# Optimization experiments

Hardware: AMD Instinct MI355X
Metric: run time of the kernel (lower is better)

Reference implementation:

```python
import jax, jax.numpy as jnp
import numpy as np

B, NK, NQ = 16, 1024, 1024
D_IN, D_V, D_H = 3, 8, 128
NUGGET = 1e-3   # diagonal regularizer for the kriging covariance solve
EPS = 1e-12     # keeps sqrt differentiable at zero distance


def _mlp(x, w1, b1, w2, b2, w3, b3):
    # Linear -> ReLU -> Linear -> ReLU -> Linear (torch Linear: y = x @ W.T + b)
    h = jax.nn.relu(x @ w1.T + b1)
    h = jax.nn.relu(h @ w2.T + b2)
    return h @ w3.T + b3


def _cdist(a, b):
    # a: [B,N,D], b: [B,M,D] -> [B,N,M] Euclidean distances
    d2 = (jnp.sum(a * a, -1)[:, :, None]
          + jnp.sum(b * b, -1)[:, None, :]
          - 2.0 * jnp.einsum('bnd,bmd->bnm', a, b))
    return jnp.sqrt(jnp.maximum(d2, 0.0) + EPS)


def _linear_init(key, out_f, in_f):
    k1, k2 = jax.random.split(key)
    lim = 1.0 / np.sqrt(in_f)
    w = jax.random.uniform(k1, (out_f, in_f), jnp.float32, -lim, lim)
    b = jax.random.uniform(k2, (out_f,), jnp.float32, -lim, lim)
    return w, b


def setup_inputs() -> dict:
    key = jax.random.key(0)
    ks = jax.random.split(key, 10)
    KEY = jax.random.normal(ks[0], (B, NK, D_IN), jnp.float32)
    VALUE = jax.random.normal(ks[1], (B, NK, D_V), jnp.float32)
    QUERY = jax.random.normal(ks[2], (B, NQ, D_IN), jnp.float32)
    W1_w, W1_b = _linear_init(ks[3], D_H, D_IN)
    W2_w, W2_b = _linear_init(ks[4], D_H, D_H)
    W3_w, W3_b = _linear_init(ks[5], D_IN, D_H)
    Wv1_w, Wv1_b = _linear_init(ks[6], D_H, D_V)
    Wv2_w, Wv2_b = _linear_init(ks[7], D_H, D_H)
    Wv3_w, Wv3_b = _linear_init(ks[8], D_V, D_H)
    return dict(KEY=KEY, VALUE=VALUE, QUERY=QUERY,
                W1_w=W1_w, W1_b=W1_b, W2_w=W2_w, W2_b=W2_b, W3_w=W3_w, W3_b=W3_b,
                Wv1_w=Wv1_w, Wv1_b=Wv1_b, Wv2_w=Wv2_w, Wv2_b=Wv2_b, Wv3_w=Wv3_w, Wv3_b=Wv3_b)


def reference(KEY, VALUE, QUERY,
              W1_w, W1_b, W2_w, W2_b, W3_w, W3_b,
              Wv1_w, Wv1_b, Wv2_w, Wv2_b, Wv3_w, Wv3_b):
    # shared MLP on KEY and QUERY, separate MLP on VALUE
    Wk = _mlp(KEY, W1_w, W1_b, W2_w, W2_b, W3_w, W3_b)
    Wq = _mlp(QUERY, W1_w, W1_b, W2_w, W2_b, W3_w, W3_b)
    Wv = _mlp(VALUE, Wv1_w, Wv1_b, Wv2_w, Wv2_b, Wv3_w, Wv3_b)
    VALUE_scale = VALUE * Wv                  # einsum('bij,bij->bij')
    # kriging prediction with learned elementwise coordinate scalings
    Ks = KEY * Wk                             # [B,NK,D_IN]
    Qs = QUERY * Wq                           # [B,NQ,D_IN]
    C_kk = jnp.exp(-_cdist(Ks, Ks)) + NUGGET * jnp.eye(NK, dtype=KEY.dtype)  # [B,NK,NK]
    C_qk = jnp.exp(-_cdist(Qs, Ks))                                          # [B,NQ,NK]
    # kriging weights: solve C_kk @ lam = C_qk^T  -> lam [B,NK,NQ]
    lam = jnp.linalg.solve(C_kk, jnp.swapaxes(C_qk, 1, 2))
    # prediction: weighted sum of scaled values -> [B,NQ,D_V]
    return jnp.einsum('bkq,bkv->bqv', lam, VALUE_scale)
```

## Files before the change

kernel.cpp:

```cpp
#include <hip/hip_runtime.h>
#include <hip/hip_bf16.h>


__device__ __forceinline__ int row_of(int e) {
    int i = (int)((sqrtf(8.0f * (float)e + 1.0f) - 1.0f) * 0.5f);
    while ((i + 1) * (i + 2) / 2 <= e) i++;
    while (i * (i + 1) / 2 > e) i--;
    return i;
}

__global__ void k_transpose(const float* __restrict__ W2, const float* __restrict__ Wv2,
                            float* __restrict__ W2T, float* __restrict__ Wv2T) {
    int tid = blockIdx.x * 256 + threadIdx.x;
    int e = tid & 16383;
    int r = e >> 7, c = e & 127;
    if (tid < 16384) W2T[c * 128 + r] = W2[e];
    else             Wv2T[c * 128 + r] = Wv2[e];
}

template<int DI, int P>
__device__ __forceinline__ void mlp_body(const float* __restrict__ in,
                                         float* __restrict__ out, int base,
                                         const float* __restrict__ W1,
                                         const float* __restrict__ b1,
                                         const float* __restrict__ W2T,
                                         const float* __restrict__ b2,
                                         const float* __restrict__ W3,
                                         const float* __restrict__ b3) {
    __shared__ float xs[P][DI];
    __shared__ float h1[P][128];
    __shared__ float h2[P][129];
    int t = threadIdx.x;
    for (int i = t; i < P * DI; i += 128) xs[i / DI][i % DI] = in[base * DI + i];
    __syncthreads();
    float w1r[DI];
#pragma unroll
    for (int d = 0; d < DI; d++) w1r[d] = W1[t * DI + d];
    float b1t = b1[t], b2t = b2[t];
#pragma unroll
    for (int p = 0; p < P; p++) {
        float s = b1t;
#pragma unroll
        for (int d = 0; d < DI; d++) s += w1r[d] * xs[p][d];
        h1[p][t] = fmaxf(s, 0.0f);
    }
    __syncthreads();
    float acc[P];
#pragma unroll
    for (int p = 0; p < P; p++) acc[p] = b2t;
    for (int k = 0; k < 128; k++) {
        float w = W2T[k * 128 + t];
#pragma unroll
        for (int p = 0; p < P; p++) acc[p] += w * h1[p][k];
    }
#pragma unroll
    for (int p = 0; p < P; p++) h2[p][t] = fmaxf(acc[p], 0.0f);
    __syncthreads();
    if (t < P * DI) {
        int p = t / DI, d = t % DI;
        float s = b3[d];
        for (int k = 0; k < 128; k++) s += W3[d * 128 + k] * h2[p][k];
        int gi = base * DI + t;
        out[gi] = in[gi] * s;
    }
}

__global__ void k_mlp_kq(const float* __restrict__ KEY, float* __restrict__ Ks,
                         const float* __restrict__ QUERY, float* __restrict__ Qs,
                         const float* __restrict__ W1, const float* __restrict__ b1,
                         const float* __restrict__ W2T, const float* __restrict__ b2,
                         const float* __restrict__ W3, const float* __restrict__ b3) {
    if (blockIdx.x < 512)
        mlp_body<3, 32>(KEY, Ks, blockIdx.x * 32, W1, b1, W2T, b2, W3, b3);
    else
        mlp_body<3, 32>(QUERY, Qs, (blockIdx.x - 512) * 32, W1, b1, W2T, b2, W3, b3);
}

__global__ void k_mlp_v(const float* __restrict__ VALUE, float* __restrict__ Vs,
                        const float* __restrict__ W1, const float* __restrict__ b1,
                        const float* __restrict__ W2T, const float* __restrict__ b2,
                        const float* __restrict__ W3, const float* __restrict__ b3) {
    mlp_body<8, 16>(VALUE, Vs, blockIdx.x * 16, W1, b1, W2T, b2, W3, b3);
}

__global__ void k_buildC(const float* __restrict__ Ks, float* __restrict__ C) {
    long idx = (long)blockIdx.x * 256 + threadIdx.x;
    int b = (int)(idx >> 20);
    int rem = (int)(idx & 1048575);
    int i = rem >> 10, j = rem & 1023;
    const float* a = Ks + ((long)b * 1024 + i) * 3;
    const float* bb = Ks + ((long)b * 1024 + j) * 3;
    float d0 = a[0] - bb[0], d1 = a[1] - bb[1], d2 = a[2] - bb[2];
    float dist = sqrtf(d0 * d0 + d1 * d1 + d2 * d2 + 1e-12f);
    float v = __expf(-dist);
    if (i == j) v += 1e-3f;
    C[idx] = v;
}

__device__ void potf_body(float* __restrict__ C, float* __restrict__ V,
                          int o, int last, int b) {
    int tid = threadIdx.x;
    float* A = C + (long)b * 1048576;
    float* Vp = V + (long)b * 8192;
    __shared__ float T[128][132];
    __shared__ __align__(16) float cv[128][8];
    __shared__ __align__(16) float cw[128][8];
    __shared__ __align__(16) float Pn[128][8];
    __shared__ __align__(16) float St[32][132];
    __shared__ float rsd[128];
    __shared__ float W[32][33];
    __shared__ float zs[128][9];
    bool active = (tid < 136);
    int ti = 0, tj = 0;
    if (active) { ti = row_of(tid); tj = tid - ti * (ti + 1) / 2; }
    int r0 = ti * 8, c0t = tj * 8;
    float Treg[8][8];
    if (active) {
        const float* src = A + (long)(o + r0) * 1024 + o + c0t;
#pragma unroll
        for (int i = 0; i < 8; i++) {
            float4 va = *(const float4*)(src + (long)i * 1024);
            float4 vb = *(const float4*)(src + (long)i * 1024 + 4);
            Treg[i][0] = va.x; Treg[i][1] = va.y; Treg[i][2] = va.z; Treg[i][3] = va.w;
            Treg[i][4] = vb.x; Treg[i][5] = vb.y; Treg[i][6] = vb.z; Treg[i][7] = vb.w;
        }
    }
    int lane = tid & 63;
    __syncthreads();
    if (o > 0) {
        for (int kc = 0; kc < 4; kc++) {
            {
                int r = tid >> 1, lk = (tid & 1) * 16;
                const float* sp = A + (long)(o + r) * 1024 + (o - 128) + kc * 32 + lk;
#pragma unroll
                for (int k4 = 0; k4 < 4; k4++) {
                    float4 v = *(const float4*)(sp + 4 * k4);
                    St[lk + 4*k4    ][r] = v.x;
                    St[lk + 4*k4 + 1][r] = v.y;
                    St[lk + 4*k4 + 2][r] = v.z;
                    St[lk + 4*k4 + 3][r] = v.w;
                }
            }
            __syncthreads();
            if (active) {
#pragma unroll 4
                for (int k = 0; k < 32; k++) {
                    float4 a0 = *(const float4*)&St[k][r0];
                    float4 a1 = *(const float4*)&St[k][r0 + 4];
                    float4 b0 = *(const float4*)&St[k][c0t];
                    float4 b1 = *(const float4*)&St[k][c0t + 4];
                    float aa[8] = {a0.x,a0.y,a0.z,a0.w,a1.x,a1.y,a1.z,a1.w};
                    float bb[8] = {b0.x,b0.y,b0.z,b0.w,b1.x,b1.y,b1.z,b1.w};
#pragma unroll
                    for (int i = 0; i < 8; i++)
#pragma unroll
                        for (int j = 0; j < 8; j++) Treg[i][j] -= aa[i] * bb[j];
                }
            }
            __syncthreads();
        }
    }
    for (int jbt = 0; jbt < 16; jbt++) {
        int jb = jbt * 8;
        if (active && tj == jbt) {
#pragma unroll
            for (int i = 0; i < 8; i++) {
                *(float4*)&Pn[r0 + i][0] = make_float4(Treg[i][0], Treg[i][1], Treg[i][2], Treg[i][3]);
                *(float4*)&Pn[r0 + i][4] = make_float4(Treg[i][4], Treg[i][5], Treg[i][6], Treg[i][7]);
            }
        }
        __syncthreads();
        if (tid < 64) {
            int r1 = lane, r2 = 64 + lane;
            float v1[8], v2[8], w1[8], w2[8];
#pragma unroll
            for (int q = 0; q < 8; q++) {
                int j = jb + q;
                int jl = j & 63;
                bool hi = (j >= 64);
                float a1 = Pn[r1][q], a2 = Pn[r2][q];
#pragma unroll
                for (int p = 0; p < 8; p++) {
                    if (p < q) {
                        float wj = __shfl(hi ? w2[p] : w1[p], jl);
                        a1 -= v1[p] * wj;
                        a2 -= v2[p] * wj;
                    }
                }
                v1[q] = a1; v2[q] = a2;
                float dj = __shfl(hi ? a2 : a1, jl);
                float dinv = 1.0f / dj;
                w1[q] = a1 * dinv; w2[q] = a2 * dinv;
            }
            *(float4*)&cv[r1][0] = make_float4(v1[0], v1[1], v1[2], v1[3]);
            *(float4*)&cv[r1][4] = make_float4(v1[4], v1[5], v1[6], v1[7]);
            *(float4*)&cv[r2][0] = make_float4(v2[0], v2[1], v2[2], v2[3]);
            *(float4*)&cv[r2][4] = make_float4(v2[4], v2[5], v2[6], v2[7]);
            *(float4*)&cw[r1][0] = make_float4(w1[0], w1[1], w1[2], w1[3]);
            *(float4*)&cw[r1][4] = make_float4(w1[4], w1[5], w1[6], w1[7]);
            *(float4*)&cw[r2][0] = make_float4(w2[0], w2[1], w2[2], w2[3]);
            *(float4*)&cw[r2][4] = make_float4(w2[4], w2[5], w2[6], w2[7]);
        }
        __syncthreads();
        if (active && tj == jbt) {
#pragma unroll
            for (int i = 0; i < 8; i++) {
                float4 va = *(const float4*)&cv[r0 + i][0];
                float4 vb = *(const float4*)&cv[r0 + i][4];
                Treg[i][0] = va.x; Treg[i][1] = va.y; Treg[i][2] = va.z; Treg[i][3] = va.w;
                Treg[i][4] = vb.x; Treg[i][5] = vb.y; Treg[i][6] = vb.z; Treg[i][7] = vb.w;
            }
        } else if (active && tj > jbt) {
#pragma unroll
            for (int h = 0; h < 2; h++) {
                float va4[8][4], wb4[8][4];
#pragma unroll
                for (int i = 0; i < 8; i++) {
                    float4 v = *(const float4*)&cv[r0 + i][h * 4];
                    va4[i][0] = v.x; va4[i][1] = v.y; va4[i][2] = v.z; va4[i][3] = v.w;
                }
#pragma unroll
                for (int j = 0; j < 8; j++) {
                    float4 v = *(const float4*)&cw[c0t + j][h * 4];
                    wb4[j][0] = v.x; wb4[j][1] = v.y; wb4[j][2] = v.z; wb4[j][3] = v.w;
                }
#pragma unroll
                for (int i = 0; i < 8; i++)
#pragma unroll
                    for (int j = 0; j < 8; j++)
                        Treg[i][j] -= va4[i][0] * wb4[j][0] + va4[i][1] * wb4[j][1]
                                    + va4[i][2] * wb4[j][2] + va4[i][3] * wb4[j][3];
            }
        }
        __syncthreads();
    }
    if (active) {
#pragma unroll
        for (int i = 0; i < 8; i++) {
            *(float4*)&T[r0 + i][c0t]     = make_float4(Treg[i][0], Treg[i][1], Treg[i][2], Treg[i][3]);
            *(float4*)&T[r0 + i][c0t + 4] = make_float4(Treg[i][4], Treg[i][5], Treg[i][6], Treg[i][7]);
        }
    }
    __syncthreads();
    int rg = tid >> 4;
    int cg = tid & 15;
    int wv = tid >> 6;
    if (tid < 128) rsd[tid] = rsqrtf(T[tid][tid]);
    __syncthreads();
#pragma unroll
    for (int j = 0; j < 8; j++) {
        int c = cg + 16 * j;
#pragma unroll
        for (int i = 0; i < 8; i++) {
            int r = rg * 8 + i;
            if (c <= r) T[r][c] *= rsd[c];
            else        T[r][c] = 0.0f;
        }
    }
    __syncthreads();
    if (lane < 32) {
        int d0 = wv * 32;
        int j = lane;
        float x[32];
#pragma unroll
        for (int i = 0; i < 32; i++) {
            float dinv = 1.0f / T[d0 + i][d0 + i];
            float s = 0.0f;
#pragma unroll
            for (int k = 0; k < i; k++) s += T[d0 + i][d0 + k] * x[k];
            x[i] = (i == j) ? dinv : -s * dinv;
        }
#pragma unroll
        for (int i = 0; i < 32; i++) T[d0 + i][d0 + j] = x[i];
    }
    __syncthreads();
    int orr = tid >> 3;
    int oc = (tid & 7) * 4;
    for (int j = 0; j < 3; j++) {
        for (int i = j + 1; i < 4; i++) {
            float w0 = 0, w1 = 0, w2 = 0, w3 = 0;
            for (int kb = j; kb < i; kb++) {
#pragma unroll 8
                for (int kk = 0; kk < 32; kk++) {
                    float l = T[i * 32 + orr][kb * 32 + kk];
                    w0 += l * T[kb * 32 + kk][j * 32 + oc    ];
                    w1 += l * T[kb * 32 + kk][j * 32 + oc + 1];
                    w2 += l * T[kb * 32 + kk][j * 32 + oc + 2];
                    w3 += l * T[kb * 32 + kk][j * 32 + oc + 3];
                }
            }
            W[orr][oc] = w0; W[orr][oc+1] = w1; W[orr][oc+2] = w2; W[orr][oc+3] = w3;
            __syncthreads();
            float v0 = 0, v1 = 0, v2 = 0, v3 = 0;
#pragma unroll 8
            for (int kk = 0; kk < 32; kk++) {
                float l = T[i * 32 + orr][i * 32 + kk];
                v0 += l * W[kk][oc    ];
                v1 += l * W[kk][oc + 1];
                v2 += l * W[kk][oc + 2];
                v3 += l * W[kk][oc + 3];
            }
            __syncthreads();
            T[i * 32 + orr][j * 32 + oc    ] = -v0;
            T[i * 32 + orr][j * 32 + oc + 1] = -v1;
            T[i * 32 + orr][j * 32 + oc + 2] = -v2;
            T[i * 32 + orr][j * 32 + oc + 3] = -v3;
            __syncthreads();
        }
    }
    {
        int r = tid >> 1, c0 = (tid & 1) * 64;
        float* dst = A + (long)(o + r) * 1024 + o + c0;
#pragma unroll
        for (int k = 0; k < 16; k++) {
            int c = c0 + 4 * k;
            float4 v = make_float4(T[r][c], T[r][c + 1], T[r][c + 2], T[r][c + 3]);
            *(float4*)(dst + 4 * k) = v;
        }
    }
    {
        int k = tid >> 1, c0 = (tid & 1) * 4;
        float4 v = *(const float4*)&Vp[(o + k) * 8 + c0];
        zs[k][c0] = v.x; zs[k][c0 + 1] = v.y; zs[k][c0 + 2] = v.z; zs[k][c0 + 3] = v.w;
    }
    __syncthreads();
    {
        int r = tid & 127, c0 = (tid >> 7) * 4;
        float y0 = 0, y1 = 0, y2 = 0, y3 = 0;
#pragma unroll 8
        for (int k = 0; k < 128; k++) {
            float l = T[r][k];
            y0 += l * zs[k][c0    ];
            y1 += l * zs[k][c0 + 1];
            y2 += l * zs[k][c0 + 2];
            y3 += l * zs[k][c0 + 3];
        }
        if (!last) {
            *(float4*)&Vp[(o + r) * 8 + c0] = make_float4(y0, y1, y2, y3);
        } else {
            __syncthreads();
            zs[r][c0] = y0; zs[r][c0+1] = y1; zs[r][c0+2] = y2; zs[r][c0+3] = y3;
            __syncthreads();
            float x0 = 0, x1 = 0, x2 = 0, x3 = 0;
#pragma unroll 8
            for (int k = 0; k < 128; k++) {
                float l = T[k][r];
                x0 += l * zs[k][c0    ];
                x1 += l * zs[k][c0 + 1];
                x2 += l * zs[k][c0 + 2];
                x3 += l * zs[k][c0 + 3];
            }
            *(float4*)&Vp[(o + r) * 8 + c0] = make_float4(x0, x1, x2, x3);
        }
    }
}

__device__ void syrk_body(float* __restrict__ C, int o, int pti, int ptj, int b) {
    float* A = C + (long)b * 1048576;
    int bi = o + 128 + pti * 128, bj = o + 128 + ptj * 128;
    __shared__ float As[32][132];
    __shared__ float Bs[32][132];
    int tid = threadIdx.x;
    int tx = tid & 15, ty = tid >> 4;
    float acc[8][8] = {};
    int lr = tid >> 1;
    int lk = (tid & 1) * 16;
    bool diag = (bi == bj);
    for (int kc = 0; kc < 128; kc += 32) {
        {
            const float* src = A + (long)(bi + lr) * 1024 + o + kc + lk;
#pragma unroll
            for (int k4 = 0; k4 < 4; k4++) {
                float4 v = *(const float4*)(src + 4 * k4);
                As[lk + 4*k4    ][lr] = v.x;
                As[lk + 4*k4 + 1][lr] = v.y;
                As[lk + 4*k4 + 2][lr] = v.z;
                As[lk + 4*k4 + 3][lr] = v.w;
            }
            if (!diag) {
                const float* sb = A + (long)(bj + lr) * 1024 + o + kc + lk;
#pragma unroll
                for (int k4 = 0; k4 < 4; k4++) {
                    float4 v = *(const float4*)(sb + 4 * k4);
                    Bs[lk + 4*k4    ][lr] = v.x;
                    Bs[lk + 4*k4 + 1][lr] = v.y;
                    Bs[lk + 4*k4 + 2][lr] = v.z;
                    Bs[lk + 4*k4 + 3][lr] = v.w;
                }
            }
        }
        __syncthreads();
        {
            const float (*Bp)[132] = diag ? As : Bs;
#pragma unroll
            for (int k = 0; k < 32; k++) {
                float4 a0 = *(const float4*)&As[k][ty * 8];
                float4 a1 = *(const float4*)&As[k][ty * 8 + 4];
                float4 b0 = *(const float4*)&Bp[k][tx * 8];
                float4 b1 = *(const float4*)&Bp[k][tx * 8 + 4];
                float aa[8] = {a0.x,a0.y,a0.z,a0.w,a1.x,a1.y,a1.z,a1.w};
                float bb[8] = {b0.x,b0.y,b0.z,b0.w,b1.x,b1.y,b1.z,b1.w};
#pragma unroll
                for (int i = 0; i < 8; i++)
#pragma unroll
                    for (int j = 0; j < 8; j++) acc[i][j] += aa[i] * bb[j];
            }
        }
        __syncthreads();
    }
#pragma unroll
    for (int i = 0; i < 8; i++) {
        int r = bi + ty * 8 + i;
        float* dst = A + (long)r * 1024 + bj + tx * 8;
        if (!diag) {
            float4 p0 = *(const float4*)dst;
            float4 p1 = *(const float4*)(dst + 4);
            p0.x -= acc[i][0]; p0.y -= acc[i][1]; p0.z -= acc[i][2]; p0.w -= acc[i][3];
            p1.x -= acc[i][4]; p1.y -= acc[i][5]; p1.z -= acc[i][6]; p1.w -= acc[i][7];
            *(float4*)dst = p0;
            *(float4*)(dst + 4) = p1;
        } else {
#pragma unroll
            for (int j = 0; j < 8; j++) {
                int c = bj + tx * 8 + j;
                if (c <= r) dst[j] -= acc[i][j];
            }
        }
    }
}

__global__ __launch_bounds__(256) void k_potf_syrk(float* __restrict__ C,
                                                   float* __restrict__ V,
                                                   int o, int last) {
    int bx = blockIdx.x;
    if (bx < 16) {
        potf_body(C, V, o, last, bx);
    } else {
        int v = bx - 16;
        int bb = v & 15;
        int p = (v >> 4) + 1;
        int tii = row_of(p);
        int tjj = p - tii * (tii + 1) / 2;
        syrk_body(C, o - 128, tii, tjj, bb);
    }
}

__global__ __launch_bounds__(256) void k_trsmg(float* __restrict__ C,
                                               float* __restrict__ V, int o) {
    int b = blockIdx.y;
    float* A = C + (long)b * 1048576;
    float* Vp = V + (long)b * 8192;
    int bi = o + 128 + blockIdx.x * 128;
    const float* Linv = A + (long)o * 1024 + o;
    __shared__ float As[32][132];
    __shared__ float Ls[32][132];
    int tid = threadIdx.x;
    int tx = tid & 15, ty = tid >> 4;
    float acc[8][8] = {};
    int lr = tid >> 1;
    int lk = (tid & 1) * 16;
    for (int kc = 0; kc < 128; kc += 32) {
        const float* src = A + (long)(bi + lr) * 1024 + o + kc + lk;
        const float* sl  = Linv + (long)lr * 1024 + kc + lk;
#pragma unroll
        for (int k4 = 0; k4 < 4; k4++) {
            float4 v = *(const float4*)(src + 4 * k4);
            As[lk + 4*k4    ][lr] = v.x;
            As[lk + 4*k4 + 1][lr] = v.y;
            As[lk + 4*k4 + 2][lr] = v.z;
            As[lk + 4*k4 + 3][lr] = v.w;
            float4 w = *(const float4*)(sl + 4 * k4);
            Ls[lk + 4*k4    ][lr] = w.x;
            Ls[lk + 4*k4 + 1][lr] = w.y;
            Ls[lk + 4*k4 + 2][lr] = w.z;
            Ls[lk + 4*k4 + 3][lr] = w.w;
        }
        __syncthreads();
#pragma unroll
        for (int k = 0; k < 32; k++) {
            float4 a0 = *(const float4*)&As[k][ty * 8];
            float4 a1 = *(const float4*)&As[k][ty * 8 + 4];
            float4 b0 = *(const float4*)&Ls[k][tx * 8];
            float4 b1 = *(const float4*)&Ls[k][tx * 8 + 4];
            float aa[8] = {a0.x,a0.y,a0.z,a0.w,a1.x,a1.y,a1.z,a1.w};
            float bb[8] = {b0.x,b0.y,b0.z,b0.w,b1.x,b1.y,b1.z,b1.w};
#pragma unroll
            for (int i = 0; i < 8; i++)
#pragma unroll
                for (int j = 0; j < 8; j++) acc[i][j] += aa[i] * bb[j];
        }
        __syncthreads();
    }
#pragma unroll
    for (int i = 0; i < 8; i++) {
        float* dst = A + (long)(bi + ty * 8 + i) * 1024 + o + tx * 8;
        *(float4*)dst       = make_float4(acc[i][0], acc[i][1], acc[i][2], acc[i][3]);
        *(float4*)(dst + 4) = make_float4(acc[i][4], acc[i][5], acc[i][6], acc[i][7]);
    }
    float* ysf = &Ls[0][0];
    {
        int k = tid >> 1, c0 = (tid & 1) * 4;
        float4 v = *(const float4*)&Vp[(o + k) * 8 + c0];
        ysf[k * 9 + c0] = v.x; ysf[k * 9 + c0 + 1] = v.y;
        ysf[k * 9 + c0 + 2] = v.z; ysf[k * 9 + c0 + 3] = v.w;
    }
    __syncthreads();
    float zacc0 = 0, zacc1 = 0, zacc2 = 0, zacc3 = 0;
    int zr = tid & 127, zc0 = (tid >> 7) * 4;
#pragma unroll
    for (int ch = 0; ch < 4; ch++) {
        if ((tx >> 2) == ch) {
            int cb = (tx & 3) * 8;
#pragma unroll
            for (int j = 0; j < 8; j++)
#pragma unroll
                for (int i = 0; i < 8; i++)
                    As[cb + j][ty * 8 + i] = acc[i][j];
        }
        __syncthreads();
#pragma unroll 8
        for (int k = 0; k < 32; k++) {
            float l = As[k][zr];
            const float* yp = &ysf[(ch * 32 + k) * 9 + zc0];
            zacc0 += l * yp[0]; zacc1 += l * yp[1];
            zacc2 += l * yp[2]; zacc3 += l * yp[3];
        }
        __syncthreads();
    }
    float* vp = &Vp[(bi + zr) * 8 + zc0];
    float4 old = *(const float4*)vp;
    old.x -= zacc0; old.y -= zacc1; old.z -= zacc2; old.w -= zacc3;
    *(float4*)vp = old;
}

__global__ __launch_bounds__(256) void k_bstep(const float* __restrict__ C,
                                               float* __restrict__ V, int k) {
    int b = blockIdx.y, j = blockIdx.x, tid = threadIdx.x;
    const float* A = C + (long)b * 1048576;
    float* Vp = V + (long)b * 8192;
    __shared__ float Lb[128][129];
    __shared__ float xs[128][9];
    __shared__ float ys[128][9];
    {
        int kk = tid >> 1, c0 = (tid & 1) * 4;
        float4 v = *(const float4*)&Vp[(k * 128 + kk) * 8 + c0];
        xs[kk][c0] = v.x; xs[kk][c0+1] = v.y; xs[kk][c0+2] = v.z; xs[kk][c0+3] = v.w;
    }
#pragma unroll
    for (int m = 0; m < 16; m++) {
        int e = tid + m * 256;
        int i = e >> 5, j4 = (e & 31) * 4;
        float4 v = *(const float4*)&A[(long)(k * 128 + i) * 1024 + j * 128 + j4];
        Lb[i][j4] = v.x; Lb[i][j4+1] = v.y; Lb[i][j4+2] = v.z; Lb[i][j4+3] = v.w;
    }
    __syncthreads();
    int r = tid & 127, c0 = (tid >> 7) * 4;
    float u0 = 0, u1 = 0, u2 = 0, u3 = 0;
#pragma unroll 8
    for (int kk = 0; kk < 128; kk++) {
        float l = Lb[kk][r];
        u0 += l * xs[kk][c0    ];
        u1 += l * xs[kk][c0 + 1];
        u2 += l * xs[kk][c0 + 2];
        u3 += l * xs[kk][c0 + 3];
    }
    float* vp = &Vp[(j * 128 + r) * 8 + c0];
    float4 old = *(const float4*)vp;
    old.x -= u0; old.y -= u1; old.z -= u2; old.w -= u3;
    if (j < k - 1) {
        *(float4*)vp = old;
    } else {
        ys[r][c0] = old.x; ys[r][c0+1] = old.y; ys[r][c0+2] = old.z; ys[r][c0+3] = old.w;
        __syncthreads();
        int o = j * 128;
#pragma unroll
        for (int m = 0; m < 16; m++) {
            int e = tid + m * 256;
            int i = e >> 5, j4 = (e & 31) * 4;
            float4 v = *(const float4*)&A[(long)(o + i) * 1024 + o + j4];
            Lb[i][j4] = v.x; Lb[i][j4+1] = v.y; Lb[i][j4+2] = v.z; Lb[i][j4+3] = v.w;
        }
        __syncthreads();
        float x0 = 0, x1 = 0, x2 = 0, x3 = 0;
#pragma unroll 8
        for (int kk = 0; kk < 128; kk++) {
            float l = Lb[kk][r];
            x0 += l * ys[kk][c0    ];
            x1 += l * ys[kk][c0 + 1];
            x2 += l * ys[kk][c0 + 2];
            x3 += l * ys[kk][c0 + 3];
        }
        *(float4*)vp = make_float4(x0, x1, x2, x3);
    }
}

__global__ void k_out(const float* __restrict__ Qs, const float* __restrict__ Ks,
                      const float* __restrict__ X, float* __restrict__ out) {
    int b = blockIdx.x >> 4;
    int qc = blockIdx.x & 15;
    int t = threadIdx.x;
    int q = t & 63, ks = t >> 6;
    __shared__ float kx[1024][3];
    __shared__ __align__(16) float xv[1024][8];
    __shared__ float red[4][64][8];
    for (int i = t; i < 3072; i += 256) kx[i / 3][i % 3] = Ks[b * 3072 + i];
    for (int i = t; i < 8192; i += 256) xv[i >> 3][i & 7] = X[b * 8192 + i];
    __syncthreads();
    int gq = b * 1024 + qc * 64 + q;
    const float* qp = Qs + (long)gq * 3;
    float qx = qp[0], qy = qp[1], qz = qp[2];
    float acc[8] = {};
    int k0 = ks * 256;
#pragma unroll 2
    for (int k = k0; k < k0 + 256; k++) {
        float dx = qx - kx[k][0], dy = qy - kx[k][1], dz = qz - kx[k][2];
        float w = __expf(-sqrtf(dx * dx + dy * dy + dz * dz + 1e-12f));
        float4 xa = *(const float4*)&xv[k][0];
        float4 xb = *(const float4*)&xv[k][4];
        acc[0] += w * xa.x; acc[1] += w * xa.y; acc[2] += w * xa.z; acc[3] += w * xa.w;
        acc[4] += w * xb.x; acc[5] += w * xb.y; acc[6] += w * xb.z; acc[7] += w * xb.w;
    }
#pragma unroll
    for (int c = 0; c < 8; c++) red[ks][q][c] = acc[c];
    __syncthreads();
    if (ks == 0) {
        float* op = out + (long)gq * 8;
#pragma unroll
        for (int c = 0; c < 8; c++)
            op[c] = red[0][q][c] + red[1][q][c] + red[2][q][c] + red[3][q][c];
    }
}

extern "C" void kernel_launch(void* const* d_in, const int* in_sizes, int n_in,
                              void* d_out, int out_size, void* d_ws, size_t ws_size,
                              hipStream_t stream) {
    const float* KEY   = (const float*)d_in[0];
    const float* VALUE = (const float*)d_in[1];
    const float* QUERY = (const float*)d_in[2];
    const float* W1w = (const float*)d_in[3];  const float* W1b = (const float*)d_in[4];
    const float* W2w = (const float*)d_in[5];  const float* W2b = (const float*)d_in[6];
    const float* W3w = (const float*)d_in[7];  const float* W3b = (const float*)d_in[8];
    const float* Wv1w = (const float*)d_in[9]; const float* Wv1b = (const float*)d_in[10];
    const float* Wv2w = (const float*)d_in[11];const float* Wv2b = (const float*)d_in[12];
    const float* Wv3w = (const float*)d_in[13];const float* Wv3b = (const float*)d_in[14];

    float* ws  = (float*)d_ws;
    float* C    = ws;
    float* Ks   = C + 16777216;
    float* Qs   = Ks + 49152;
    float* Vs   = Qs + 49152;
    float* W2T  = Vs + 131072;
    float* Wv2T = W2T + 16384;

    float* out = (float*)d_out;

    hipLaunchKernelGGL(k_transpose, dim3(128), dim3(256), 0, stream, W2w, Wv2w, W2T, Wv2T);
    hipLaunchKernelGGL(k_mlp_kq, dim3(1024), dim3(128), 0, stream,
                       KEY, Ks, QUERY, Qs, W1w, W1b, W2T, W2b, W3w, W3b);
    hipLaunchKernelGGL(k_mlp_v, dim3(1024), dim3(128), 0, stream,
                       VALUE, Vs, Wv1w, Wv1b, Wv2T, Wv2b, Wv3w, Wv3b);
    hipLaunchKernelGGL(k_buildC, dim3(65536), dim3(256), 0, stream, Ks, C);

    for (int s = 0; s < 8; s++) {
        int o = s * 128;
        int np = 0;
        if (s >= 1) { int ntp = 8 - s; np = ntp * (ntp + 1) / 2 - 1; }
        hipLaunchKernelGGL(k_potf_syrk, dim3(16 + np * 16), dim3(256), 0, stream,
                           C, Vs, o, (s == 7) ? 1 : 0);
        int nt = 7 - s;
        if (nt > 0)
            hipLaunchKernelGGL(k_trsmg, dim3(nt, 16), dim3(256), 0, stream, C, Vs, o);
    }
    for (int k = 7; k >= 1; k--)
        hipLaunchKernelGGL(k_bstep, dim3(k, 16), dim3(256), 0, stream, C, Vs, k);

    hipLaunchKernelGGL(k_out, dim3(256), dim3(256), 0, stream, Qs, Ks, Vs, out);
}
```

Before: 1.138 ms.

## Double threads in fused Cholesky panel/SYRK kernel with double-buffered staging

Raises the fused POTRF/SYRK kernel from 256 to 512 threads. Each thread now owns half a tile (4x8 instead of 8x8), which spreads the panel factorization and SYRK update over more lanes and lowers register pressure. The trailing-update staging buffer is double-buffered to drop a barrier per chunk. The diagonal Pn write is moved into the previous update step. The block inversion gains a second team that computes independent off-diagonal inverse blocks, using a copied block cache (Lc). The costs are a larger shared-memory footprint in one unioned buffer, more complex index logic, and more threads that sit idle in the serial 64-lane column sweep.

```diff
diff --git a/kernel.cpp b/kernel.cpp
--- a/kernel.cpp
+++ b/kernel.cpp
@@ -98,78 +98,87 @@
 }
 
 __device__ void potf_body(float* __restrict__ C, float* __restrict__ V,
-                          int o, int last, int b) {
+                          float* smem, int o, int last, int b) {
     int tid = threadIdx.x;
     float* A = C + (long)b * 1048576;
     float* Vp = V + (long)b * 8192;
-    __shared__ float T[128][132];
-    __shared__ __align__(16) float cv[128][8];
-    __shared__ __align__(16) float cw[128][8];
-    __shared__ __align__(16) float Pn[128][8];
-    __shared__ __align__(16) float St[32][132];
-    __shared__ float rsd[128];
-    __shared__ float W[32][33];
-    __shared__ float zs[128][9];
-    bool active = (tid < 136);
-    int ti = 0, tj = 0;
-    if (active) { ti = row_of(tid); tj = tid - ti * (ti + 1) / 2; }
-    int r0 = ti * 8, c0t = tj * 8;
-    float Treg[8][8];
+    float (*T)[132]      = (float(*)[132])smem;
+    float (*cv)[8]       = (float(*)[8])(smem + 16896);
+    float (*cw)[8]       = (float(*)[8])(smem + 17920);
+    float (*Pn)[8]       = (float(*)[8])(smem + 18944);
+    float (*St)[32][132] = (float(*)[32][132])(smem + 19968);
+    float (*Lc)[32][33]  = (float(*)[32][33])(smem + 19968);
+    float* rsd           = smem + 28416;
+    float (*Wb)[32][33]  = (float(*)[32][33])(smem + 28544);
+    float (*zs)[9]       = (float(*)[9])(smem + 30656);
+
+    bool active = (tid < 272);
+    int ti = 0, tj = 0, hh = 0;
+    if (active) { int e = tid >> 1; hh = tid & 1; ti = row_of(e); tj = e - ti * (ti + 1) / 2; }
+    int r0 = ti * 8 + hh * 4, c0t = tj * 8;
+    int lane = tid & 63;
+    int sr = tid >> 2, slk = (tid & 3) * 8;
+
+    if (o > 0) {
+        const float* sp = A + (long)(o + sr) * 1024 + (o - 128) + slk;
+        float4 v0 = *(const float4*)sp;
+        float4 v1 = *(const float4*)(sp + 4);
+        St[0][slk    ][sr] = v0.x; St[0][slk + 1][sr] = v0.y;
+        St[0][slk + 2][sr] = v0.z; St[0][slk + 3][sr] = v0.w;
+        St[0][slk + 4][sr] = v1.x; St[0][slk + 5][sr] = v1.y;
+        St[0][slk + 6][sr] = v1.z; St[0][slk + 7][sr] = v1.w;
+    }
+    float Treg[4][8];
     if (active) {
         const float* src = A + (long)(o + r0) * 1024 + o + c0t;
 #pragma unroll
-        for (int i = 0; i < 8; i++) {
+        for (int i = 0; i < 4; i++) {
             float4 va = *(const float4*)(src + (long)i * 1024);
             float4 vb = *(const float4*)(src + (long)i * 1024 + 4);
             Treg[i][0] = va.x; Treg[i][1] = va.y; Treg[i][2] = va.z; Treg[i][3] = va.w;
             Treg[i][4] = vb.x; Treg[i][5] = vb.y; Treg[i][6] = vb.z; Treg[i][7] = vb.w;
         }
     }
-    int lane = tid & 63;
-    __syncthreads();
     if (o > 0) {
         for (int kc = 0; kc < 4; kc++) {
-            {
-                int r = tid >> 1, lk = (tid & 1) * 16;
-                const float* sp = A + (long)(o + r) * 1024 + (o - 128) + kc * 32 + lk;
-#pragma unroll
-                for (int k4 = 0; k4 < 4; k4++) {
-                    float4 v = *(const float4*)(sp + 4 * k4);
-                    St[lk + 4*k4    ][r] = v.x;
-                    St[lk + 4*k4 + 1][r] = v.y;
-                    St[lk + 4*k4 + 2][r] = v.z;
-                    St[lk + 4*k4 + 3][r] = v.w;
-                }
-            }
             __syncthreads();
+            if (kc < 3) {
+                const float* sp = A + (long)(o + sr) * 1024 + (o - 128) + (kc + 1) * 32 + slk;
+                float4 v0 = *(const float4*)sp;
+                float4 v1 = *(const float4*)(sp + 4);
+                int nb = (kc + 1) & 1;
+                St[nb][slk    ][sr] = v0.x; St[nb][slk + 1][sr] = v0.y;
+                St[nb][slk + 2][sr] = v0.z; St[nb][slk + 3][sr] = v0.w;
+                St[nb][slk + 4][sr] = v1.x; St[nb][slk + 5][sr] = v1.y;
+                St[nb][slk + 6][sr] = v1.z; St[nb][slk + 7][sr] = v1.w;
+            }
             if (active) {
+                int buf = kc & 1;
 #pragma unroll 4
                 for (int k = 0; k < 32; k++) {
-                    float4 a0 = *(const float4*)&St[k][r0];
-                    float4 a1 = *(const float4*)&St[k][r0 + 4];
-                    float4 b0 = *(const float4*)&St[k][c0t];
-                    float4 b1 = *(const float4*)&St[k][c0t + 4];
-                    float aa[8] = {a0.x,a0.y,a0.z,a0.w,a1.x,a1.y,a1.z,a1.w};
-                    float bb[8] = {b0.x,b0.y,b0.z,b0.w,b1.x,b1.y,b1.z,b1.w};
-#pragma unroll
-                    for (int i = 0; i < 8; i++)
+                    float4 a0 = *(const float4*)&St[buf][k][r0];
+                    float4 b0 = *(const float4*)&St[buf][k][c0t];
+                    float4 b1 = *(const float4*)&St[buf][k][c0t + 4];
+                    float aa[4] = {a0.x, a0.y, a0.z, a0.w};
+                    float bb[8] = {b0.x, b0.y, b0.z, b0.w, b1.x, b1.y, b1.z, b1.w};
+#pragma unroll
+                    for (int i = 0; i < 4; i++)
 #pragma unroll
                         for (int j = 0; j < 8; j++) Treg[i][j] -= aa[i] * bb[j];
                 }
             }
-            __syncthreads();
-        }
-    }
+        }
+    }
+    if (active && tj == 0) {
+#pragma unroll
+        for (int i = 0; i < 4; i++) {
+            *(float4*)&Pn[r0 + i][0] = make_float4(Treg[i][0], Treg[i][1], Treg[i][2], Treg[i][3]);
+            *(float4*)&Pn[r0 + i][4] = make_float4(Treg[i][4], Treg[i][5], Treg[i][6], Treg[i][7]);
+        }
+    }
+    __syncthreads();
     for (int jbt = 0; jbt < 16; jbt++) {
         int jb = jbt * 8;
-        if (active && tj == jbt) {
-#pragma unroll
-            for (int i = 0; i < 8; i++) {
-                *(float4*)&Pn[r0 + i][0] = make_float4(Treg[i][0], Treg[i][1], Treg[i][2], Treg[i][3]);
-                *(float4*)&Pn[r0 + i][4] = make_float4(Treg[i][4], Treg[i][5], Treg[i][6], Treg[i][7]);
-            }
-        }
-        __syncthreads();
         if (tid < 64) {
             int r1 = lane, r2 = 64 + lane;
             float v1[8], v2[8], w1[8], w2[8];
@@ -204,7 +213,7 @@
         __syncthreads();
         if (active && tj == jbt) {
 #pragma unroll
-            for (int i = 0; i < 8; i++) {
+            for (int i = 0; i < 4; i++) {
                 float4 va = *(const float4*)&cv[r0 + i][0];
                 float4 vb = *(const float4*)&cv[r0 + i][4];
                 Treg[i][0] = va.x; Treg[i][1] = va.y; Treg[i][2] = va.z; Treg[i][3] = va.w;
@@ -213,9 +222,9 @@
         } else if (active && tj > jbt) {
 #pragma unroll
             for (int h = 0; h < 2; h++) {
-                float va4[8][4], wb4[8][4];
-#pragma unroll
-                for (int i = 0; i < 8; i++) {
+                float va4[4][4], wb4[8][4];
+#pragma unroll
+                for (int i = 0; i < 4; i++) {
                     float4 v = *(const float4*)&cv[r0 + i][h * 4];
                     va4[i][0] = v.x; va4[i][1] = v.y; va4[i][2] = v.z; va4[i][3] = v.w;
                 }
@@ -225,183 +234,199 @@
                     wb4[j][0] = v.x; wb4[j][1] = v.y; wb4[j][2] = v.z; wb4[j][3] = v.w;
                 }
 #pragma unroll
-                for (int i = 0; i < 8; i++)
+                for (int i = 0; i < 4; i++)
 #pragma unroll
                     for (int j = 0; j < 8; j++)
                         Treg[i][j] -= va4[i][0] * wb4[j][0] + va4[i][1] * wb4[j][1]
                                     + va4[i][2] * wb4[j][2] + va4[i][3] * wb4[j][3];
             }
+            if (tj == jbt + 1) {
+#pragma unroll
+                for (int i = 0; i < 4; i++) {
+                    *(float4*)&Pn[r0 + i][0] = make_float4(Treg[i][0], Treg[i][1], Treg[i][2], Treg[i][3]);
+                    *(float4*)&Pn[r0 + i][4] = make_float4(Treg[i][4], Treg[i][5], Treg[i][6], Treg[i][7]);
+                }
+            }
         }
         __syncthreads();
     }
     if (active) {
 #pragma unroll
-        for (int i = 0; i < 8; i++) {
+        for (int i = 0; i < 4; i++) {
             *(float4*)&T[r0 + i][c0t]     = make_float4(Treg[i][0], Treg[i][1], Treg[i][2], Treg[i][3]);
             *(float4*)&T[r0 + i][c0t + 4] = make_float4(Treg[i][4], Treg[i][5], Treg[i][6], Treg[i][7]);
         }
     }
     __syncthreads();
-    int rg = tid >> 4;
-    int cg = tid & 15;
-    int wv = tid >> 6;
     if (tid < 128) rsd[tid] = rsqrtf(T[tid][tid]);
     __syncthreads();
-#pragma unroll
-    for (int j = 0; j < 8; j++) {
-        int c = cg + 16 * j;
-#pragma unroll
-        for (int i = 0; i < 8; i++) {
-            int r = rg * 8 + i;
-            if (c <= r) T[r][c] *= rsd[c];
-            else        T[r][c] = 0.0f;
-        }
-    }
-    __syncthreads();
-    if (lane < 32) {
-        int d0 = wv * 32;
-        int j = lane;
-        float x[32];
-#pragma unroll
-        for (int i = 0; i < 32; i++) {
-            float dinv = 1.0f / T[d0 + i][d0 + i];
-            float s = 0.0f;
-#pragma unroll
-            for (int k = 0; k < i; k++) s += T[d0 + i][d0 + k] * x[k];
-            x[i] = (i == j) ? dinv : -s * dinv;
-        }
-#pragma unroll
-        for (int i = 0; i < 32; i++) T[d0 + i][d0 + j] = x[i];
-    }
-    __syncthreads();
-    int orr = tid >> 3;
-    int oc = (tid & 7) * 4;
-    for (int j = 0; j < 3; j++) {
-        for (int i = j + 1; i < 4; i++) {
+    {
+        int rg = tid >> 5, cg = tid & 31;
+#pragma unroll
+        for (int j = 0; j < 4; j++) {
+            int c = cg + 32 * j;
+#pragma unroll
+            for (int i = 0; i < 8; i++) {
+                int r = rg * 8 + i;
+                if (c <= r) T[r][c] *= rsd[c];
+                else        T[r][c] = 0.0f;
+            }
+        }
+    }
+    __syncthreads();
+    {
+        int wv = tid >> 6;
+        if (wv < 4 && lane < 32) {
+            int d0 = wv * 32;
+            int j = lane;
+            float x[32];
+#pragma unroll
+            for (int i = 0; i < 32; i++) {
+                float dinv = 1.0f / T[d0 + i][d0 + i];
+                float s = 0.0f;
+#pragma unroll
+                for (int k = 0; k < i; k++) s += T[d0 + i][d0 + k] * x[k];
+                x[i] = (i == j) ? dinv : -s * dinv;
+            }
+#pragma unroll
+            for (int i = 0; i < 32; i++) T[d0 + i][d0 + j] = x[i];
+        }
+        if (tid >= 256) {
+            for (int idx = tid - 256; idx < 6144; idx += 256) {
+                int p = idx >> 10;
+                int e = idx & 1023;
+                int r = e >> 5, c = e & 31;
+                int i3 = (p == 0) ? 1 : (p <= 2 ? 2 : 3);
+                int kb = (p == 0) ? 0 : (p <= 2 ? p - 1 : p - 3);
+                Lc[p][r][c] = T[i3 * 32 + r][kb * 32 + c];
+            }
+        }
+    }
+    __syncthreads();
+    {
+        int team = tid >> 8, ttid = tid & 255;
+        int orr = ttid >> 3, oc = (ttid & 7) * 4;
+        for (int st = 0; st < 3; st++) {
+            int i3, j3;
+            if (team == 0) { i3 = st + 1; j3 = 0; }
+            else           { i3 = (st == 0) ? 2 : 3; j3 = (st == 2) ? 2 : 1; }
             float w0 = 0, w1 = 0, w2 = 0, w3 = 0;
-            for (int kb = j; kb < i; kb++) {
+            for (int kb = j3; kb < i3; kb++) {
+                int p = i3 * (i3 - 1) / 2 + kb;
 #pragma unroll 8
                 for (int kk = 0; kk < 32; kk++) {
-                    float l = T[i * 32 + orr][kb * 32 + kk];
-                    w0 += l * T[kb * 32 + kk][j * 32 + oc    ];
-                    w1 += l * T[kb * 32 + kk][j * 32 + oc + 1];
-                    w2 += l * T[kb * 32 + kk][j * 32 + oc + 2];
-                    w3 += l * T[kb * 32 + kk][j * 32 + oc + 3];
+                    float l = Lc[p][orr][kk];
+                    w0 += l * T[kb * 32 + kk][j3 * 32 + oc    ];
+                    w1 += l * T[kb * 32 + kk][j3 * 32 + oc + 1];
+                    w2 += l * T[kb * 32 + kk][j3 * 32 + oc + 2];
+                    w3 += l * T[kb * 32 + kk][j3 * 32 + oc + 3];
                 }
             }
-            W[orr][oc] = w0; W[orr][oc+1] = w1; W[orr][oc+2] = w2; W[orr][oc+3] = w3;
+            Wb[team][orr][oc] = w0; Wb[team][orr][oc + 1] = w1;
+            Wb[team][orr][oc + 2] = w2; Wb[team][orr][oc + 3] = w3;
             __syncthreads();
             float v0 = 0, v1 = 0, v2 = 0, v3 = 0;
 #pragma unroll 8
             for (int kk = 0; kk < 32; kk++) {
-                float l = T[i * 32 + orr][i * 32 + kk];
-                v0 += l * W[kk][oc    ];
-                v1 += l * W[kk][oc + 1];
-                v2 += l * W[kk][oc + 2];
-                v3 += l * W[kk][oc + 3];
+                float l = T[i3 * 32 + orr][i3 * 32 + kk];
+                v0 += l * Wb[team][kk][oc    ];
+                v1 += l * Wb[team][kk][oc + 1];
+                v2 += l * Wb[team][kk][oc + 2];
+                v3 += l * Wb[team][kk][oc + 3];
             }
             __syncthreads();
-            T[i * 32 + orr][j * 32 + oc    ] = -v0;
-            T[i * 32 + orr][j * 32 + oc + 1] = -v1;
-            T[i * 32 + orr][j * 32 + oc + 2] = -v2;
-            T[i * 32 + orr][j * 32 + oc + 3] = -v3;
+            T[i3 * 32 + orr][j3 * 32 + oc    ] = -v0;
+            T[i3 * 32 + orr][j3 * 32 + oc + 1] = -v1;
+            T[i3 * 32 + orr][j3 * 32 + oc + 2] = -v2;
+            T[i3 * 32 + orr][j3 * 32 + oc + 3] = -v3;
             __syncthreads();
         }
     }
     {
-        int r = tid >> 1, c0 = (tid & 1) * 64;
+        int r = tid >> 2, c0 = (tid & 3) * 32;
         float* dst = A + (long)(o + r) * 1024 + o + c0;
 #pragma unroll
-        for (int k = 0; k < 16; k++) {
+        for (int k = 0; k < 8; k++) {
             int c = c0 + 4 * k;
-            float4 v = make_float4(T[r][c], T[r][c + 1], T[r][c + 2], T[r][c + 3]);
-            *(float4*)(dst + 4 * k) = v;
+            *(float4*)(dst + 4 * k) = make_float4(T[r][c], T[r][c + 1], T[r][c + 2], T[r][c + 3]);
         }
     }
     {
-        int k = tid >> 1, c0 = (tid & 1) * 4;
-        float4 v = *(const float4*)&Vp[(o + k) * 8 + c0];
-        zs[k][c0] = v.x; zs[k][c0 + 1] = v.y; zs[k][c0 + 2] = v.z; zs[k][c0 + 3] = v.w;
+        int k = tid >> 2, c2 = (tid & 3) * 2;
+        float2 v = *(const float2*)&Vp[(o + k) * 8 + c2];
+        zs[k][c2] = v.x; zs[k][c2 + 1] = v.y;
     }
     __syncthreads();
     {
-        int r = tid & 127, c0 = (tid >> 7) * 4;
-        float y0 = 0, y1 = 0, y2 = 0, y3 = 0;
+        int r = tid & 127, c2 = (tid >> 7) * 2;
+        float y0 = 0, y1 = 0;
 #pragma unroll 8
         for (int k = 0; k < 128; k++) {
             float l = T[r][k];
-            y0 += l * zs[k][c0    ];
-            y1 += l * zs[k][c0 + 1];
-            y2 += l * zs[k][c0 + 2];
-            y3 += l * zs[k][c0 + 3];
+            y0 += l * zs[k][c2];
+            y1 += l * zs[k][c2 + 1];
         }
         if (!last) {
-            *(float4*)&Vp[(o + r) * 8 + c0] = make_float4(y0, y1, y2, y3);
+            *(float2*)&Vp[(o + r) * 8 + c2] = make_float2(y0, y1);
         } else {
             __syncthreads();
-            zs[r][c0] = y0; zs[r][c0+1] = y1; zs[r][c0+2] = y2; zs[r][c0+3] = y3;
+            zs[r][c2] = y0; zs[r][c2 + 1] = y1;
             __syncthreads();
-            float x0 = 0, x1 = 0, x2 = 0, x3 = 0;
+            float x0 = 0, x1 = 0;
 #pragma unroll 8
             for (int k = 0; k < 128; k++) {
                 float l = T[k][r];
-                x0 += l * zs[k][c0    ];
-                x1 += l * zs[k][c0 + 1];
-                x2 += l * zs[k][c0 + 2];
-                x3 += l * zs[k][c0 + 3];
-            }
-            *(float4*)&Vp[(o + r) * 8 + c0] = make_float4(x0, x1, x2, x3);
-        }
-    }
-}
-
-__device__ void syrk_body(float* __restrict__ C, int o, int pti, int ptj, int b) {
+                x0 += l * zs[k][c2];
+                x1 += l * zs[k][c2 + 1];
+            }
+            *(float2*)&Vp[(o + r) * 8 + c2] = make_float2(x0, x1);
+        }
+    }
+}
+
+__device__ void syrk_body(float* __restrict__ C, float* smem,
+                          int o, int pti, int ptj, int b) {
     float* A = C + (long)b * 1048576;
     int bi = o + 128 + pti * 128, bj = o + 128 + ptj * 128;
-    __shared__ float As[32][132];
-    __shared__ float Bs[32][132];
+    float (*As)[132] = (float(*)[132])smem;
+    float (*Bs)[132] = (float(*)[132])(smem + 4224);
     int tid = threadIdx.x;
     int tx = tid & 15, ty = tid >> 4;
-    float acc[8][8] = {};
-    int lr = tid >> 1;
-    int lk = (tid & 1) * 16;
+    float acc[4][8] = {};
+    int lr = tid >> 2;
+    int lk = (tid & 3) * 8;
     bool diag = (bi == bj);
     for (int kc = 0; kc < 128; kc += 32) {
         {
             const float* src = A + (long)(bi + lr) * 1024 + o + kc + lk;
-#pragma unroll
-            for (int k4 = 0; k4 < 4; k4++) {
-                float4 v = *(const float4*)(src + 4 * k4);
-                As[lk + 4*k4    ][lr] = v.x;
-                As[lk + 4*k4 + 1][lr] = v.y;
-                As[lk + 4*k4 + 2][lr] = v.z;
-                As[lk + 4*k4 + 3][lr] = v.w;
-            }
+            float4 v0 = *(const float4*)src;
+            float4 v1 = *(const float4*)(src + 4);
+            As[lk    ][lr] = v0.x; As[lk + 1][lr] = v0.y;
+            As[lk + 2][lr] = v0.z; As[lk + 3][lr] = v0.w;
+            As[lk + 4][lr] = v1.x; As[lk + 5][lr] = v1.y;
+            As[lk + 6][lr] = v1.z; As[lk + 7][lr] = v1.w;
             if (!diag) {
                 const float* sb = A + (long)(bj + lr) * 1024 + o + kc + lk;
-#pragma unroll
-                for (int k4 = 0; k4 < 4; k4++) {
-                    float4 v = *(const float4*)(sb + 4 * k4);
-                    Bs[lk + 4*k4    ][lr] = v.x;
-                    Bs[lk + 4*k4 + 1][lr] = v.y;
-                    Bs[lk + 4*k4 + 2][lr] = v.z;
-                    Bs[lk + 4*k4 + 3][lr] = v.w;
-                }
+                float4 w0 = *(const float4*)sb;
+                float4 w1 = *(const float4*)(sb + 4);
+                Bs[lk    ][lr] = w0.x; Bs[lk + 1][lr] = w0.y;
+                Bs[lk + 2][lr] = w0.z; Bs[lk + 3][lr] = w0.w;
+                Bs[lk + 4][lr] = w1.x; Bs[lk + 5][lr] = w1.y;
+                Bs[lk + 6][lr] = w1.z; Bs[lk + 7][lr] = w1.w;
             }
         }
         __syncthreads();
         {
-            const float (*Bp)[132] = diag ? As : Bs;
+            float (*Bp)[132] = diag ? As : Bs;
 #pragma unroll
             for (int k = 0; k < 32; k++) {
-                float4 a0 = *(const float4*)&As[k][ty * 8];
-                float4 a1 = *(const float4*)&As[k][ty * 8 + 4];
+                float4 a0 = *(const float4*)&As[k][ty * 4];
                 float4 b0 = *(const float4*)&Bp[k][tx * 8];
                 float4 b1 = *(const float4*)&Bp[k][tx * 8 + 4];
-                float aa[8] = {a0.x,a0.y,a0.z,a0.w,a1.x,a1.y,a1.z,a1.w};
-                float bb[8] = {b0.x,b0.y,b0.z,b0.w,b1.x,b1.y,b1.z,b1.w};
-#pragma unroll
-                for (int i = 0; i < 8; i++)
+                float aa[4] = {a0.x, a0.y, a0.z, a0.w};
+                float bb[8] = {b0.x, b0.y, b0.z, b0.w, b1.x, b1.y, b1.z, b1.w};
+#pragma unroll
+                for (int i = 0; i < 4; i++)
 #pragma unroll
                     for (int j = 0; j < 8; j++) acc[i][j] += aa[i] * bb[j];
             }
@@ -409,8 +434,8 @@
         __syncthreads();
     }
 #pragma unroll
-    for (int i = 0; i < 8; i++) {
-        int r = bi + ty * 8 + i;
+    for (int i = 0; i < 4; i++) {
+        int r = bi + ty * 4 + i;
         float* dst = A + (long)r * 1024 + bj + tx * 8;
         if (!diag) {
             float4 p0 = *(const float4*)dst;
@@ -429,19 +454,20 @@
     }
 }
 
-__global__ __launch_bounds__(256) void k_potf_syrk(float* __restrict__ C,
+__global__ __launch_bounds__(512) void k_potf_syrk(float* __restrict__ C,
                                                    float* __restrict__ V,
                                                    int o, int last) {
+    __shared__ __align__(16) float smem[31808];
     int bx = blockIdx.x;
     if (bx < 16) {
-        potf_body(C, V, o, last, bx);
+        potf_body(C, V, smem, o, last, bx);
     } else {
         int v = bx - 16;
         int bb = v & 15;
         int p = (v >> 4) + 1;
         int tii = row_of(p);
         int tjj = p - tii * (tii + 1) / 2;
-        syrk_body(C, o - 128, tii, tjj, bb);
+        syrk_body(C, smem, o - 128, tii, tjj, bb);
     }
 }
 
@@ -665,7 +691,7 @@
         int o = s * 128;
         int np = 0;
         if (s >= 1) { int ntp = 8 - s; np = ntp * (ntp + 1) / 2 - 1; }
-        hipLaunchKernelGGL(k_potf_syrk, dim3(16 + np * 16), dim3(256), 0, stream,
+        hipLaunchKernelGGL(k_potf_syrk, dim3(16 + np * 16), dim3(512), 0, stream,
                            C, Vs, o, (s == 7) ? 1 : 0);
         int nt = 7 - s;
         if (nt > 0)
```

Measured after the change: 998.5 us. 1.14x faster.
